# Kernel tuning notes

Measured on AMD Instinct MI355X. Metric: run time of the kernel, lower is better.

The kernel has to match this reference:

```python
import jax, jax.numpy as jnp
import numpy as np

B, C, H, W = 64, 3, 512, 512
KSIZE = 13
EPS = 8.0
IDENTITY_OFFSET = 4.0
DEFORM_OFFSET = (2.0 + IDENTITY_OFFSET / (W - 1)) / 2.0
SCALE_X = IDENTITY_OFFSET / (W - 1)
SCALE_Y = IDENTITY_OFFSET / (H - 1)


def setup_inputs() -> dict:
    key = jax.random.key(0)
    k1, k2 = jax.random.split(key)
    image = jax.random.uniform(k1, (B, C, H, W), dtype=jnp.float32)
    prim_grid = jax.random.normal(k2, (B, 2, H, W), dtype=jnp.float32) * 0.01
    return {"image": image, "prim_grid": prim_grid}


def _samp_iden():
    seq = jnp.arange(-(W - 1), W, 2, dtype=jnp.float32) / (W - 1)
    gx = jnp.broadcast_to(seq[None, :], (H, W))
    gy = gx.T
    return jnp.stack([gx, gy], axis=0)[None]  # [1,2,H,W]


def _gaussian_blur(x, ksize):
    sigma = ksize * 0.15 + 0.35
    half = (ksize - 1) * 0.5
    t = jnp.linspace(-half, half, ksize)
    pdf = jnp.exp(-0.5 * (t / sigma) ** 2)
    k1 = pdf / pdf.sum()
    k2d = jnp.outer(k1, k1)
    p = ksize // 2
    xp = jnp.pad(x, ((0, 0), (0, 0), (p, p), (p, p)), mode='reflect')
    kernel = jnp.broadcast_to(k2d[None, None], (2, 1, ksize, ksize))
    return jax.lax.conv_general_dilated(
        xp, kernel, window_strides=(1, 1), padding='VALID',
        feature_group_count=2, dimension_numbers=('NCHW', 'OIHW', 'NCHW'))


def _samp2accu(samp):
    # conv_transpose with [1,-1] kernel + crop == first-difference with zero prepend
    s = samp + DEFORM_OFFSET
    ax = jnp.diff(s[:, 0:1], axis=3, prepend=jnp.zeros_like(s[:, 0:1, :, :1])) / SCALE_X
    ay = jnp.diff(s[:, 1:2], axis=2, prepend=jnp.zeros_like(s[:, 1:2, :1, :])) / SCALE_Y
    return jnp.concatenate([ax, ay], axis=1)


def _accu2samp(accu):
    # conv_transpose with full-ones kernel + crop == cumulative sum
    sx = jnp.cumsum(accu[:, 0:1] * SCALE_X, axis=3)
    sy = jnp.cumsum(accu[:, 1:2] * SCALE_Y, axis=2)
    return jnp.concatenate([sx, sy], axis=1) - DEFORM_OFFSET


def _grid_sample(image, grid):
    # image [B,C,H,W], grid [B,H,W,2] xy in [-1,1], bilinear, align_corners=True, zeros pad
    gx = (grid[..., 0] + 1.0) * 0.5 * (W - 1)
    gy = (grid[..., 1] + 1.0) * 0.5 * (H - 1)
    x0 = jnp.floor(gx)
    y0 = jnp.floor(gy)
    wx = gx - x0
    wy = gy - y0
    x0i = x0.astype(jnp.int32)
    x1i = x0i + 1
    y0i = y0.astype(jnp.int32)
    y1i = y0i + 1

    def gather(img, yi, xi):
        valid = ((xi >= 0) & (xi < W) & (yi >= 0) & (yi < H)).astype(img.dtype)
        xc = jnp.clip(xi, 0, W - 1)
        yc = jnp.clip(yi, 0, H - 1)
        return img[:, yc, xc] * valid[None]  # [C,H,W]

    def per_b(img, y0i, y1i, x0i, x1i, wx, wy):
        v00 = gather(img, y0i, x0i)
        v01 = gather(img, y0i, x1i)
        v10 = gather(img, y1i, x0i)
        v11 = gather(img, y1i, x1i)
        return (v00 * (1 - wx) * (1 - wy) + v01 * wx * (1 - wy)
                + v10 * (1 - wx) * wy + v11 * wx * wy)

    return jax.vmap(per_b)(image, y0i, y1i, x0i, x1i, wx, wy)


def _forward_grid(prim_grid):
    iden = _samp_iden()
    p = _gaussian_blur(prim_grid, KSIZE)
    accu = jnp.maximum(_samp2accu(p + iden), 0.0)          # accu_clip (relu)
    p = _accu2samp(accu) - iden
    bound = (2.0 / W) * EPS
    p = jnp.clip(p, -bound, bound)                          # prim_clip
    samp = jnp.clip(p + iden, -1.0, 1.0)                    # samp_clip (hardtanh)
    return samp


def reference(image, prim_grid):
    samp = _forward_grid(prim_grid)
    grid = jnp.transpose(samp, (0, 2, 3, 1))  # [B,H,W,2]
    return _grid_sample(image, grid)
```

## Files before the change

kernel.cpp:

```cpp
#include <hip/hip_runtime.h>
#include <math.h>

#define HH 512
#define WW 512
#define NB 64
#define HW (HH*WW)

struct GaussK { float k[13]; };

__device__ __forceinline__ float idenv(int i) {
    return (float)(2*i - (WW-1)) / (float)(WW-1);
}

#define DEF_OFF ((float)((2.0 + 4.0/511.0)/2.0))
#define BOUND   ((float)(2.0/512.0*8.0))

typedef float vf2 __attribute__((ext_vector_type(2), aligned(4)));

__device__ __forceinline__ void hconv_row(const float (&a)[8], int lane, const GaussK& gk, float (&o)[8]) {
    float win[20];
    #pragma unroll
    for (int i = 0; i < 6; ++i) {
        float v = __shfl_up(a[i+2], 1, 64);
        win[i] = (lane == 0) ? a[6-i] : v;
    }
    #pragma unroll
    for (int i = 6; i < 14; ++i) win[i] = a[i-6];
    #pragma unroll
    for (int i = 14; i < 20; ++i) {
        float v = __shfl_down(a[i-14], 1, 64);
        win[i] = (lane == 63) ? a[20-i] : v;
    }
    #pragma unroll
    for (int j = 0; j < 8; ++j) {
        float acc = 0.f;
        #pragma unroll
        for (int i = 0; i < 13; ++i) acc = fmaf(gk.k[i], win[j+i], acc);
        o[j] = acc;
    }
}

__device__ __forceinline__ void xscan_row(const float (&a)[8], int lane, const GaussK& gk, float* row0) {
    float win[21];
    #pragma unroll
    for (int i = 0; i < 7; ++i) {
        float v = __shfl_up(a[i+1], 1, 64);
        win[i] = (lane == 0) ? a[7-i] : v;
    }
    #pragma unroll
    for (int i = 0; i < 8; ++i) win[7+i] = a[i];
    #pragma unroll
    for (int i = 15; i < 21; ++i) {
        float v = __shfl_down(a[i-15], 1, 64);
        win[i] = (lane == 63) ? a[21-i] : v;
    }
    float s[9];
    #pragma unroll
    for (int j = 0; j < 9; ++j) {
        float acc = 0.f;
        #pragma unroll
        for (int i = 0; i < 13; ++i) acc = fmaf(gk.k[i], win[j+i], acc);
        s[j] = acc + idenv(8*lane - 1 + j) + DEF_OFF;
    }
    if (lane == 0) s[0] = 0.f;

    float qs[8], q = 0.f;
    #pragma unroll
    for (int j = 1; j < 9; ++j) { q += fmaxf(s[j] - s[j-1], 0.f); qs[j-1] = q; }
    float inc = q;
    #pragma unroll
    for (int d = 1; d < 64; d <<= 1) {
        float t = __shfl_up(inc, d, 64);
        if (lane >= d) inc += t;
    }
    float excl = inc - q;

    float4 g0, g1;
    float* gp0 = (float*)&g0;
    float* gp1 = (float*)&g1;
    #pragma unroll
    for (int j = 0; j < 8; ++j) {
        int wcol = lane*8 + j;
        float sx = excl + qs[j];
        float p = sx - DEF_OFF - idenv(wcol);
        p = fminf(fmaxf(p, -BOUND), BOUND);
        float g = p + idenv(wcol);
        g = fminf(fmaxf(g, -1.f), 1.f);
        if (j < 4) gp0[j] = g; else gp1[j-4] = g;
    }
    *(float4*)(row0 + lane*8)     = g0;
    *(float4*)(row0 + lane*8 + 4) = g1;
}

__global__ void __launch_bounds__(256) k_prep(const float* __restrict__ prim, float* __restrict__ out, GaussK gk) {
    int lane = threadIdx.x & 63;
    int bid  = (int)blockIdx.x;
    int work = (bid & 7)*512 + (bid >> 3);
    int gw   = work*4 + ((int)threadIdx.x >> 6);
    int b    = gw >> 8;
    int h0   = (gw & 255)*2;

    const float4* src0 = (const float4*)(prim + (size_t)b*2*HW);
    const float*  src1 = prim + ((size_t)b*2 + 1)*HW;
    float* plane0 = out + (size_t)b*3*HW;
    float* plane1 = out + ((size_t)b*3 + 1)*HW;

    float a0[8] = {0,0,0,0,0,0,0,0};
    float a1[8] = {0,0,0,0,0,0,0,0};
    #pragma unroll
    for (int i = 0; i < 14; ++i) {
        int r = h0 - 6 + i;
        r = r < 0 ? -r : (r > HH-1 ? 2*(HH-1) - r : r);
        float4 u0 = src0[(size_t)r*128 + 2*lane];
        float4 u1 = src0[(size_t)r*128 + 2*lane + 1];
        float vv[8] = {u0.x,u0.y,u0.z,u0.w,u1.x,u1.y,u1.z,u1.w};
        if (i < 13) {
            #pragma unroll
            for (int j = 0; j < 8; ++j) a0[j] = fmaf(gk.k[i], vv[j], a0[j]);
        }
        if (i >= 1) {
            #pragma unroll
            for (int j = 0; j < 8; ++j) a1[j] = fmaf(gk.k[i-1], vv[j], a1[j]);
        }
    }

    #pragma unroll
    for (int r = 0; r < 2; ++r) {
        const float4* c4 = (const float4*)(src1 + (size_t)(h0+r)*WW);
        float4 u0 = c4[2*lane];
        float4 u1 = c4[2*lane + 1];
        float c[8] = {u0.x,u0.y,u0.z,u0.w,u1.x,u1.y,u1.z,u1.w};
        float o[8];
        hconv_row(c, lane, gk, o);
        float* row1 = plane1 + (size_t)(h0+r)*WW;
        *(float4*)(row1 + lane*8)     = make_float4(o[0],o[1],o[2],o[3]);
        *(float4*)(row1 + lane*8 + 4) = make_float4(o[4],o[5],o[6],o[7]);
    }

    xscan_row(a0, lane, gk, plane0 + (size_t)h0*WW);
    xscan_row(a1, lane, gk, plane0 + (size_t)(h0+1)*WW);
}

__global__ void __launch_bounds__(1024) k_yscan(float* __restrict__ out, GaussK gk) {
    __shared__ float segsum[16][64];
    int b    = blockIdx.x >> 3;
    int wt   = blockIdx.x & 7;
    int lane = threadIdx.x & 63;
    int ws   = threadIdx.x >> 6;
    int w    = wt*64 + lane;
    const float* p1 = out + ((size_t)b*3 + 1)*HW + w;
    float*       p2 = out + ((size_t)b*3 + 2)*HW + w;
    int r0 = ws*32;

    float v[45];
    #pragma unroll
    for (int j = 0; j < 45; ++j) {
        int r = r0 - 7 + j;
        r = r < 0 ? -r : (r > HH-1 ? 2*(HH-1) - r : r);
        v[j] = p1[(size_t)r*WW];
    }

    float sprev;
    if (ws == 0) {
        sprev = 0.f;
    } else {
        float acc = 0.f;
        #pragma unroll
        for (int i = 0; i < 13; ++i) acc = fmaf(gk.k[i], v[i], acc);
        sprev = acc + idenv(r0 - 1) + DEF_OFF;
    }

    float q[32];
    float run = 0.f;
    #pragma unroll
    for (int n = 0; n < 32; ++n) {
        float acc = 0.f;
        #pragma unroll
        for (int i = 0; i < 13; ++i) acc = fmaf(gk.k[i], v[n+1+i], acc);
        float s = acc + idenv(r0 + n) + DEF_OFF;
        run += fmaxf(s - sprev, 0.f);
        q[n] = run;
        sprev = s;
    }
    segsum[ws][lane] = run;
    __syncthreads();
    float off = 0.f;
    for (int k = 0; k < ws; ++k) off += segsum[k][lane];

    #pragma unroll
    for (int n = 0; n < 32; ++n) {
        int h = r0 + n;
        float p = off + q[n] - DEF_OFF - idenv(h);
        p = fminf(fmaxf(p, -BOUND), BOUND);
        float g = p + idenv(h);
        g = fminf(fmaxf(g, -1.f), 1.f);
        p2[(size_t)h*WW] = g;
    }
}

__global__ void __launch_bounds__(256) k_sample(const float* __restrict__ image, float* __restrict__ out) {
    int bid  = (int)blockIdx.x;
    int work = (bid & 7)*4096 + (bid >> 3);
    int idx  = work*256 + threadIdx.x;
    int w  = idx & (WW-1);
    int h  = (idx >> 9) & (HH-1);
    int b0 = idx >> 18;
    int off = h*WW + w;

    #pragma unroll
    for (int u = 0; u < 2; ++u) {
        int b = b0 + 32*u;
        float* ob = out + (size_t)b*3*HW;
        const float* ib = image + (size_t)b*3*HW;
        float gx = ob[off];
        float gy = ob[2*HW + off];
        float fx = (gx + 1.f) * 0.5f * (float)(WW-1);
        float fy = (gy + 1.f) * 0.5f * (float)(HH-1);
        float x0f = floorf(fx), y0f = floorf(fy);
        float wx = fx - x0f, wy = fy - y0f;
        int x0 = (int)x0f, y0 = (int)y0f;
        int y1 = y0 + 1; if (y1 > HH-1) y1 = HH-1;
        bool sh = x0 > WW-2;
        int xb = sh ? WW-2 : x0;
        size_t r0 = (size_t)y0*WW + xb;
        size_t r1 = (size_t)y1*WW + xb;
        float w11 = wx*wy;
        float w01 = wx - w11;
        float w10 = wy - w11;
        float w00 = 1.f - wx - wy + w11;
        #pragma unroll
        for (int c = 0; c < 3; ++c) {
            const float* ip = ib + (size_t)c*HW;
            vf2 t  = *(const vf2*)(ip + r0);
            vf2 bo = *(const vf2*)(ip + r1);
            float a00 = sh ? t.y  : t.x;
            float a10 = sh ? bo.y : bo.x;
            float r = a00*w00 + t.y*w01 + a10*w10 + bo.y*w11;
            __builtin_nontemporal_store(r, ob + (size_t)c*HW + off);
        }
    }
}

extern "C" void kernel_launch(void* const* d_in, const int* in_sizes, int n_in,
                              void* d_out, int out_size, void* d_ws, size_t ws_size,
                              hipStream_t stream) {
    const float* image = (const float*)d_in[0];
    const float* prim  = (const float*)d_in[1];
    float* out = (float*)d_out;

    GaussK gk;
    {
        double sigma = 13.0*0.15 + 0.35;
        double pdf[13], sum = 0.0;
        for (int i = 0; i < 13; ++i) {
            double t = (double)(i - 6);
            pdf[i] = exp(-0.5*(t/sigma)*(t/sigma));
            sum += pdf[i];
        }
        for (int i = 0; i < 13; ++i) gk.k[i] = (float)(pdf[i]/sum);
    }

    k_prep  <<<4096,           256, 0, stream>>>(prim, out, gk);
    k_yscan <<<NB*8,          1024, 0, stream>>>(out, gk);
    k_sample<<<NB*HH*WW/2/256, 256, 0, stream>>>(image, out);
}
```

Before: 251.5 us.

## Fuse vertical scan with bilinear sampling into one kernel

Merges the y-direction scan and grid-sample kernels, so each thread samples the image right after computing its y-coordinate instead of writing it to the output plane and reading it back. This removes one launch and a full-plane write and read of the intermediate y-grid. In exchange, sampling now runs inside the register-heavy 1024-thread scan blocks, with 32 serial rows per thread. That can lower occupancy and hide gather latency less well than the old dedicated kernel. Blocks only read channel 1 before the barrier and overwrite it after, so the fusion stays correct.

```diff
diff --git a/kernel.cpp b/kernel.cpp
--- a/kernel.cpp
+++ b/kernel.cpp
@@ -141,7 +141,7 @@
     xscan_row(a1, lane, gk, plane0 + (size_t)(h0+1)*WW);
 }
 
-__global__ void __launch_bounds__(1024) k_yscan(float* __restrict__ out, GaussK gk) {
+__global__ void __launch_bounds__(1024) k_yssamp(const float* __restrict__ image, float* __restrict__ out, GaussK gk) {
     __shared__ float segsum[16][64];
     int b    = blockIdx.x >> 3;
     int wt   = blockIdx.x & 7;
@@ -149,7 +149,6 @@
     int ws   = threadIdx.x >> 6;
     int w    = wt*64 + lane;
     const float* p1 = out + ((size_t)b*3 + 1)*HW + w;
-    float*       p2 = out + ((size_t)b*3 + 2)*HW + w;
     int r0 = ws*32;
 
     float v[45];
@@ -187,43 +186,29 @@
     float off = 0.f;
     for (int k = 0; k < ws; ++k) off += segsum[k][lane];
 
+    const float* ib = image + (size_t)b*3*HW;
+    float*       ob = out   + (size_t)b*3*HW;
+
     #pragma unroll
     for (int n = 0; n < 32; ++n) {
         int h = r0 + n;
+        size_t poff = (size_t)h*WW + w;
         float p = off + q[n] - DEF_OFF - idenv(h);
         p = fminf(fmaxf(p, -BOUND), BOUND);
-        float g = p + idenv(h);
-        g = fminf(fmaxf(g, -1.f), 1.f);
-        p2[(size_t)h*WW] = g;
-    }
-}
-
-__global__ void __launch_bounds__(256) k_sample(const float* __restrict__ image, float* __restrict__ out) {
-    int bid  = (int)blockIdx.x;
-    int work = (bid & 7)*4096 + (bid >> 3);
-    int idx  = work*256 + threadIdx.x;
-    int w  = idx & (WW-1);
-    int h  = (idx >> 9) & (HH-1);
-    int b0 = idx >> 18;
-    int off = h*WW + w;
-
-    #pragma unroll
-    for (int u = 0; u < 2; ++u) {
-        int b = b0 + 32*u;
-        float* ob = out + (size_t)b*3*HW;
-        const float* ib = image + (size_t)b*3*HW;
-        float gx = ob[off];
-        float gy = ob[2*HW + off];
+        float gy = p + idenv(h);
+        gy = fminf(fmaxf(gy, -1.f), 1.f);
+        float gx = ob[poff];
+
         float fx = (gx + 1.f) * 0.5f * (float)(WW-1);
         float fy = (gy + 1.f) * 0.5f * (float)(HH-1);
         float x0f = floorf(fx), y0f = floorf(fy);
         float wx = fx - x0f, wy = fy - y0f;
         int x0 = (int)x0f, y0 = (int)y0f;
         int y1 = y0 + 1; if (y1 > HH-1) y1 = HH-1;
-        bool sh = x0 > WW-2;
-        int xb = sh ? WW-2 : x0;
-        size_t r0 = (size_t)y0*WW + xb;
-        size_t r1 = (size_t)y1*WW + xb;
+        bool shx = x0 > WW-2;
+        int xb = shx ? WW-2 : x0;
+        size_t g0 = (size_t)y0*WW + xb;
+        size_t g1 = (size_t)y1*WW + xb;
         float w11 = wx*wy;
         float w01 = wx - w11;
         float w10 = wy - w11;
@@ -231,12 +216,12 @@
         #pragma unroll
         for (int c = 0; c < 3; ++c) {
             const float* ip = ib + (size_t)c*HW;
-            vf2 t  = *(const vf2*)(ip + r0);
-            vf2 bo = *(const vf2*)(ip + r1);
-            float a00 = sh ? t.y  : t.x;
-            float a10 = sh ? bo.y : bo.x;
+            vf2 t  = *(const vf2*)(ip + g0);
+            vf2 bo = *(const vf2*)(ip + g1);
+            float a00 = shx ? t.y  : t.x;
+            float a10 = shx ? bo.y : bo.x;
             float r = a00*w00 + t.y*w01 + a10*w10 + bo.y*w11;
-            __builtin_nontemporal_store(r, ob + (size_t)c*HW + off);
+            __builtin_nontemporal_store(r, ob + (size_t)c*HW + poff);
         }
     }
 }
@@ -260,7 +245,6 @@
         for (int i = 0; i < 13; ++i) gk.k[i] = (float)(pdf[i]/sum);
     }
 
-    k_prep  <<<4096,           256, 0, stream>>>(prim, out, gk);
-    k_yscan <<<NB*8,          1024, 0, stream>>>(out, gk);
-    k_sample<<<NB*HH*WW/2/256, 256, 0, stream>>>(image, out);
-}
+    k_prep  <<<4096, 256,  0, stream>>>(prim, out, gk);
+    k_yssamp<<<NB*8, 1024, 0, stream>>>(image, out, gk);
+}
```

After: 244.8 us. -2.7%, faster.
